# Performance work log

Hardware: AMD Instinct MI355X
Metric: run time of the kernel (lower is better)

Reference implementation:

```python
import jax, jax.numpy as jnp
import numpy as np

H = 16
D_MODEL = 1024
D_K = D_MODEL // H


def setup_inputs() -> dict:
    key = jax.random.key(0)
    ks = jax.random.split(key, 11)
    B, S = 2, 2048
    scale = 1.0 / np.sqrt(D_MODEL)
    inp = {
        "query": jax.random.normal(ks[0], (B, S, D_MODEL), dtype=jnp.float32),
        "key": jax.random.normal(ks[1], (B, S, D_MODEL), dtype=jnp.float32),
        "value": jax.random.normal(ks[2], (B, S, D_MODEL), dtype=jnp.float32),
        "Wq": jax.random.normal(ks[3], (D_MODEL, D_MODEL), dtype=jnp.float32) * scale,
        "bq": jnp.zeros((D_MODEL,), dtype=jnp.float32),
        "Wk": jax.random.normal(ks[4], (D_MODEL, D_MODEL), dtype=jnp.float32) * scale,
        "bk": jnp.zeros((D_MODEL,), dtype=jnp.float32),
        "Wv": jax.random.normal(ks[5], (D_MODEL, D_MODEL), dtype=jnp.float32) * scale,
        "bv": jnp.zeros((D_MODEL,), dtype=jnp.float32),
        "Wo": jax.random.normal(ks[6], (D_MODEL, D_MODEL), dtype=jnp.float32) * scale,
        "bo": jnp.zeros((D_MODEL,), dtype=jnp.float32),
    }
    return inp


def _mha(query, key, value, Wq, bq, Wk, bk, Wv, bv, Wo, bo):
    B, S, _ = query.shape
    # linear projections (torch nn.Linear: x @ W.T + b)
    q = query @ Wq.T + bq
    k = key @ Wk.T + bk
    v = value @ Wv.T + bv
    # split heads: [B, S, D] -> [B, H, S, d_k]
    q = q.reshape(B, S, H, D_K).transpose(0, 2, 1, 3)
    k = k.reshape(B, S, H, D_K).transpose(0, 2, 1, 3)
    v = v.reshape(B, S, H, D_K).transpose(0, 2, 1, 3)
    # scaled dot-product attention with manual stable softmax
    scores = jnp.einsum("bhqd,bhkd->bhqk", q, k) / jnp.sqrt(jnp.float32(D_K))
    stable = scores - jnp.max(scores, axis=-1, keepdims=True)
    e = jnp.exp(stable)
    attn = e / jnp.sum(e, axis=-1, keepdims=True)
    ctx = jnp.einsum("bhqk,bhkd->bhqd", attn, v)
    # merge heads and final projection
    ctx = ctx.transpose(0, 2, 1, 3).reshape(B, S, H * D_K)
    return ctx @ Wo.T + bo


def reference(query, key, value, Wq, bq, Wk, bk, Wv, bv, Wo, bo):
    return _mha(query, key, value, Wq, bq, Wk, bk, Wv, bv, Wo, bo)
```

## Files before the change

### kernel.cpp

```cpp
#include <hip/hip_runtime.h>


#define S_LEN 2048
#define BATCH 2
#define DM    1024
#define NH    16
#define DKH   64
#define BS    (BATCH * S_LEN)

typedef _Float16 f16x8 __attribute__((ext_vector_type(8)));
typedef _Float16 f16x4 __attribute__((ext_vector_type(4)));
typedef _Float16 f16x2 __attribute__((ext_vector_type(2)));
typedef __fp16   h16x2 __attribute__((ext_vector_type(2)));
typedef float    f32x4 __attribute__((ext_vector_type(4)));
typedef float    f32x16 __attribute__((ext_vector_type(16)));

__device__ __forceinline__ f16x2 pk_f16(float a, float b) {
  h16x2 r = __builtin_amdgcn_cvt_pkrtz(a, b);
  return __builtin_bit_cast(f16x2, r);
}

__device__ __forceinline__ void gld16(const void* g, void* l) {
  __builtin_amdgcn_global_load_lds(
      (const __attribute__((address_space(1))) void*)g,
      (__attribute__((address_space(3))) void*)l, 16, 0, 0);
}

__device__ __forceinline__ float fast_exp2(float x) {
#if __has_builtin(__builtin_amdgcn_exp2f)
  return __builtin_amdgcn_exp2f(x);
#else
  return exp2f(x);
#endif
}

__device__ __forceinline__ int swap23(int x) {
  return (x & ~12) | ((x & 4) << 1) | ((x & 8) >> 1);
}

__global__ __launch_bounds__(256) void cvt_all(
    const float* __restrict__ q, const float* __restrict__ k, const float* __restrict__ v,
    const float* __restrict__ wq, const float* __restrict__ wk,
    const float* __restrict__ wv, const float* __restrict__ wo,
    _Float16* __restrict__ xq, _Float16* __restrict__ xk, _Float16* __restrict__ xv,
    _Float16* __restrict__ w16)
{
  const int y = blockIdx.y;
  const float* src; _Float16* dst; int n;
  if (y == 0)      { src = q;  dst = xq; n = BS * DM; }
  else if (y == 1) { src = k;  dst = xk; n = BS * DM; }
  else if (y == 2) { src = v;  dst = xv; n = BS * DM; }
  else {
    src = (y == 3) ? wq : ((y == 4) ? wk : ((y == 5) ? wv : wo));
    dst = w16 + (size_t)(y - 3) * (DM * DM);
    n = DM * DM;
  }
  int i0 = (blockIdx.x * 256 + threadIdx.x) * 4;
  if (i0 < n) {
    float4 f = *(const float4*)(src + i0);
    f16x2 lo = pk_f16(f.x, f.y);
    f16x2 hi = pk_f16(f.z, f.w);
    f16x4 hh; hh[0] = lo[0]; hh[1] = lo[1]; hh[2] = hi[0]; hh[3] = hi[1];
    *(f16x4*)(dst + i0) = hh;
  }
}

template <typename OUT_T, bool VT>
__device__ __forceinline__ void gemm_core(
    const _Float16* __restrict__ A, const _Float16* __restrict__ W,
    const float* __restrict__ bias, OUT_T* __restrict__ out, float oscale)
{
  const int tid  = threadIdx.x;
  const int l    = tid & 63;
  const int wv   = tid >> 6;
  const int c    = l & 15, quad = l >> 4;
  const int m0   = blockIdx.y * 128, n0 = blockIdx.x * 128;
  const int wm   = wv & 1, wn = wv >> 1;
  __shared__ _Float16 sA[128 * 64];
  __shared__ _Float16 sB[128 * 64];

  const _Float16* gA[4]; const _Float16* gB[4];
#pragma unroll
  for (int p = 0; p < 4; ++p) {
    int s = tid + p * 256, r = s >> 3, g = (s & 7) ^ (r & 7);
    gA[p] = A + (size_t)(m0 + r) * DM + g * 8;
    gB[p] = W + (size_t)(n0 + r) * DM + g * 8;
  }
  const int cx = c & 7;

  f32x4 acc[4][4] = {};
  for (int k0 = 0; k0 < DM; k0 += 64) {
    __syncthreads();
#pragma unroll
    for (int p = 0; p < 4; ++p) {
      gld16(gA[p] + k0, sA + (tid + p * 256) * 8);
      gld16(gB[p] + k0, sB + (tid + p * 256) * 8);
    }
    __syncthreads();
#pragma unroll
    for (int ks = 0; ks < 2; ++ks) {
      f16x8 af[4], bf[4];
#pragma unroll
      for (int i = 0; i < 4; ++i)
        af[i] = *(const f16x8*)&sA[(wm * 64 + i * 16 + c) * 64 + ((ks * 4 + quad) ^ cx) * 8];
#pragma unroll
      for (int j = 0; j < 4; ++j)
        bf[j] = *(const f16x8*)&sB[(wn * 64 + j * 16 + c) * 64 + ((ks * 4 + quad) ^ cx) * 8];
#pragma unroll
      for (int i = 0; i < 4; ++i)
#pragma unroll
        for (int j = 0; j < 4; ++j)
          acc[i][j] = __builtin_amdgcn_mfma_f32_16x16x32_f16(af[i], bf[j], acc[i][j], 0, 0, 0);
    }
  }
  if constexpr (VT) {
#pragma unroll
    for (int j = 0; j < 4; ++j) {
      int col = n0 + wn * 64 + j * 16 + c;
      float bb = bias[col];
      int hh = col >> 6, dd = col & 63;
#pragma unroll
      for (int i = 0; i < 4; ++i) {
        int row = m0 + wm * 64 + i * 16 + quad * 4;
        int bb2 = row >> 11, ss = row & (S_LEN - 1);
        _Float16* dst = (_Float16*)out + ((size_t)(bb2 * NH + hh) * DKH + dd) * S_LEN + ss;
        f16x4 v4;
#pragma unroll
        for (int r = 0; r < 4; ++r) v4[r] = (_Float16)((acc[i][j][r] + bb) * oscale);
        *(f16x4*)dst = v4;
      }
    }
  } else {
#pragma unroll
    for (int j = 0; j < 4; ++j) {
      int col = n0 + wn * 64 + j * 16 + c;
      float bb = bias[col];
#pragma unroll
      for (int i = 0; i < 4; ++i) {
        int row = m0 + wm * 64 + i * 16 + quad * 4;
#pragma unroll
        for (int r = 0; r < 4; ++r) {
          float vv = (acc[i][j][r] + bb) * oscale;
          out[(size_t)(row + r) * DM + col] = (OUT_T)vv;
        }
      }
    }
  }
}

#define SC_Q (0.125f * 1.44269504088896340736f)

__global__ __launch_bounds__(256) void proj3(
    const _Float16* __restrict__ xq, const _Float16* __restrict__ xk,
    const _Float16* __restrict__ xv, const _Float16* __restrict__ w16,
    const float* __restrict__ bq, const float* __restrict__ bk, const float* __restrict__ bv,
    _Float16* __restrict__ Q, _Float16* __restrict__ K, _Float16* __restrict__ Vt)
{
  const int z = blockIdx.z;
  if (z == 2) {
    gemm_core<_Float16, true>(xv, w16 + (size_t)2 * DM * DM, bv, Vt, 1.0f);
  } else if (z == 0) {
    gemm_core<_Float16, false>(xq, w16, bq, Q, SC_Q);
  } else {
    gemm_core<_Float16, false>(xk, w16 + (size_t)DM * DM, bk, K, 1.0f);
  }
}

__global__ __launch_bounds__(256) void out_gemm(
    const _Float16* __restrict__ ctx, const _Float16* __restrict__ wo,
    const float* __restrict__ bo, float* __restrict__ out)
{
  gemm_core<float, false>(ctx, wo, bo, out, 1.0f);
}

__global__ __launch_bounds__(256, 2) void attn(
    const _Float16* __restrict__ Q, const _Float16* __restrict__ K,
    const _Float16* __restrict__ Vt, _Float16* __restrict__ ctx)
{
  const int tid = threadIdx.x;
  const int l   = tid & 63, wv = tid >> 6;
  const int lo5 = l & 31, hf = l >> 5;
  const int q0  = blockIdx.x * 128;
  const int bh  = blockIdx.y;
  const int b   = bh >> 4, hd = bh & 15;
  __shared__ _Float16 sK[3][64 * 64];
  __shared__ _Float16 sV[3][64 * 64];

  f16x8 qf[4];
  {
    const _Float16* Qg = Q + ((size_t)(b * S_LEN + q0 + wv * 32 + lo5)) * DM + hd * DKH + 8 * hf;
#pragma unroll
    for (int kc = 0; kc < 4; ++kc) qf[kc] = *(const f16x8*)(Qg + 16 * kc);
  }

  f32x16 o[2] = {};
  float l_part = 0.f;
  const f16x2 ones = {(_Float16)1.0f, (_Float16)1.0f};

  const _Float16* Kg0 = K + ((size_t)b * S_LEN) * DM + hd * DKH;
  const _Float16* Vg0 = Vt + ((size_t)bh * DKH) * S_LEN;

  const int sa = tid,       ra = sa >> 3, ba = (sa & 7) ^ (ra & 7);
  const int sb = tid + 256, rb = sb >> 3, bb = (sb & 7) ^ (rb & 7);
  const _Float16* gKa = Kg0 + (size_t)swap23(ra) * DM + ba * 8;
  const _Float16* gKb = Kg0 + (size_t)swap23(rb) * DM + bb * 8;
  const _Float16* gVa = Vg0 + (size_t)ra * S_LEN + ba * 8;
  const _Float16* gVb = Vg0 + (size_t)rb * S_LEN + bb * 8;
  const int rx = lo5 & 7;

#define STAGE(t, bf) do {                                   \
    const size_t k0s = (size_t)(t) * 64;                    \
    gld16(gKa + k0s * DM, sK[bf] + sa * 8);                 \
    gld16(gKb + k0s * DM, sK[bf] + sb * 8);                 \
    gld16(gVa + k0s,      sV[bf] + sa * 8);                 \
    gld16(gVb + k0s,      sV[bf] + sb * 8);                 \
  } while (0)

  STAGE(0, 0);
  STAGE(1, 1);

  int cur = 0;
  for (int kt = 0; kt < S_LEN / 64; ++kt) {
    if (kt == S_LEN / 64 - 1)
      asm volatile("s_waitcnt vmcnt(0)" ::: "memory");
    else
      asm volatile("s_waitcnt vmcnt(4)" ::: "memory");
    __builtin_amdgcn_s_barrier();
    if (kt < S_LEN / 64 - 2) {
      int nb = cur + 2; if (nb >= 3) nb -= 3;
      STAGE(kt + 2, nb);
    }

    const _Float16* sKc = sK[cur];
    const _Float16* sVc = sV[cur];

    f32x16 sAcc[2] = {};
    __builtin_amdgcn_s_setprio(1);
#pragma unroll
    for (int kb = 0; kb < 2; ++kb)
#pragma unroll
      for (int kc = 0; kc < 4; ++kc) {
        f16x8 kf = *(const f16x8*)&sKc[(32 * kb + lo5) * 64 + ((2 * kc + hf) ^ rx) * 8];
        sAcc[kb] = __builtin_amdgcn_mfma_f32_32x32x16_f16(kf, qf[kc], sAcc[kb], 0, 0, 0);
      }
    __builtin_amdgcn_s_setprio(0);

    f16x8 pPv[2][2];
#pragma unroll
    for (int kb = 0; kb < 2; ++kb)
#pragma unroll
      for (int half = 0; half < 2; ++half)
#pragma unroll
        for (int j2 = 0; j2 < 4; ++j2) {
          float p0 = fast_exp2(sAcc[kb][8 * half + 2 * j2]);
          float p1 = fast_exp2(sAcc[kb][8 * half + 2 * j2 + 1]);
          f16x2 pk = pk_f16(p0, p1);
          pPv[kb][half][2 * j2]     = pk[0];
          pPv[kb][half][2 * j2 + 1] = pk[1];
          l_part = __builtin_amdgcn_fdot2(__builtin_bit_cast(h16x2, pk),
                                          __builtin_bit_cast(h16x2, ones), l_part, false);
        }

    __builtin_amdgcn_s_setprio(1);
#pragma unroll
    for (int db = 0; db < 2; ++db)
#pragma unroll
      for (int kc2 = 0; kc2 < 4; ++kc2) {
        f16x8 vf = *(const f16x8*)&sVc[(32 * db + lo5) * 64 + ((2 * kc2 + hf) ^ rx) * 8];
        o[db] = __builtin_amdgcn_mfma_f32_32x32x16_f16(pPv[kc2 >> 1][kc2 & 1], vf, o[db], 0, 0, 0);
      }
    __builtin_amdgcn_s_setprio(0);

    cur = (cur == 2) ? 0 : cur + 1;
  }
#undef STAGE

  l_part += __shfl_xor(l_part, 32);
  float* lsum = (float*)&sK[0][0] + wv * 32;
  if (hf == 0) lsum[lo5] = l_part;
  float inv[16];
#pragma unroll
  for (int r = 0; r < 16; ++r) {
    int qq = 8 * (r >> 2) + 4 * hf + (r & 3);
    inv[r] = 1.0f / lsum[qq];
  }

  _Float16* Og = ctx + ((size_t)(b * S_LEN + q0 + wv * 32)) * DM + hd * DKH;
#pragma unroll
  for (int db = 0; db < 2; ++db)
#pragma unroll
    for (int r = 0; r < 16; ++r) {
      int qq = 8 * (r >> 2) + 4 * hf + (r & 3);
      Og[(size_t)qq * DM + 32 * db + lo5] = (_Float16)(o[db][r] * inv[r]);
    }
}

extern "C" void kernel_launch(void* const* d_in, const int* in_sizes, int n_in,
                              void* d_out, int out_size, void* d_ws, size_t ws_size,
                              hipStream_t stream)
{
  (void)in_sizes; (void)n_in; (void)out_size; (void)ws_size;
  const float* q  = (const float*)d_in[0];
  const float* k  = (const float*)d_in[1];
  const float* v  = (const float*)d_in[2];
  const float* wq = (const float*)d_in[3];
  const float* bq = (const float*)d_in[4];
  const float* wk = (const float*)d_in[5];
  const float* bk = (const float*)d_in[6];
  const float* wv = (const float*)d_in[7];
  const float* bv = (const float*)d_in[8];
  const float* wo = (const float*)d_in[9];
  const float* bo = (const float*)d_in[10];

  char* ws = (char*)d_ws;
  _Float16* XQ  = (_Float16*)(ws);
  _Float16* XK  = (_Float16*)(ws + (8u  << 20));
  _Float16* XV  = (_Float16*)(ws + (16u << 20));
  _Float16* W16 = (_Float16*)(ws + (24u << 20));
  _Float16* Qp  = (_Float16*)(ws + (32u << 20));
  _Float16* Kp  = (_Float16*)(ws + (40u << 20));
  _Float16* VT  = (_Float16*)(ws + (48u << 20));
  _Float16* CTX = XQ;
  float* out = (float*)d_out;

  cvt_all<<<dim3(4096, 7), 256, 0, stream>>>(q, k, v, wq, wk, wv, wo, XQ, XK, XV, W16);
  proj3<<<dim3(8, 32, 3), 256, 0, stream>>>(XQ, XK, XV, W16, bq, bk, bv, Qp, Kp, VT);
  attn<<<dim3(16, 32), 256, 0, stream>>>(Qp, Kp, VT, CTX);
  out_gemm<<<dim3(8, 32), 256, 0, stream>>>(CTX, W16 + (size_t)3 * DM * DM, bo, out);
}
```

Measured before the change: 229.7 us.

## Split attention key tiles across warp pairs and halve query block size

Each attention block now covers 64 queries instead of 128. The four waves are arranged as two query-halves times two key-halves, and each wave handles 32 of the 64 keys in every tile. The partial outputs and row sums of the two key-half waves are combined through shared memory at the end. This doubles the grid to 1024 blocks and raises the occupancy target, aiming to fill the 256 CUs better. In exchange, K/V tiles are loaded twice as often per query, the triple buffer becomes a double buffer with a full wait each iteration, and a reduction epilogue is added.

```diff
diff --git a/kernel.cpp b/kernel.cpp
--- a/kernel.cpp
+++ b/kernel.cpp
@@ -173,22 +173,23 @@
   gemm_core<float, false>(ctx, wo, bo, out, 1.0f);
 }
 
-__global__ __launch_bounds__(256, 2) void attn(
+__global__ __launch_bounds__(256, 4) void attn(
     const _Float16* __restrict__ Q, const _Float16* __restrict__ K,
     const _Float16* __restrict__ Vt, _Float16* __restrict__ ctx)
 {
   const int tid = threadIdx.x;
   const int l   = tid & 63, wv = tid >> 6;
   const int lo5 = l & 31, hf = l >> 5;
-  const int q0  = blockIdx.x * 128;
+  const int wq  = wv >> 1, wk = wv & 1;
+  const int q0  = blockIdx.x * 64;
   const int bh  = blockIdx.y;
   const int b   = bh >> 4, hd = bh & 15;
-  __shared__ _Float16 sK[3][64 * 64];
-  __shared__ _Float16 sV[3][64 * 64];
+  __shared__ _Float16 sK[2][64 * 64];
+  __shared__ _Float16 sV[2][64 * 64];
 
   f16x8 qf[4];
   {
-    const _Float16* Qg = Q + ((size_t)(b * S_LEN + q0 + wv * 32 + lo5)) * DM + hd * DKH + 8 * hf;
+    const _Float16* Qg = Q + ((size_t)(b * S_LEN + q0 + wq * 32 + lo5)) * DM + hd * DKH + 8 * hf;
 #pragma unroll
     for (int kc = 0; kc < 4; ++kc) qf[kc] = *(const f16x8*)(Qg + 16 * kc);
   }
@@ -217,82 +218,88 @@
   } while (0)
 
   STAGE(0, 0);
-  STAGE(1, 1);
-
-  int cur = 0;
-  for (int kt = 0; kt < S_LEN / 64; ++kt) {
-    if (kt == S_LEN / 64 - 1)
-      asm volatile("s_waitcnt vmcnt(0)" ::: "memory");
-    else
-      asm volatile("s_waitcnt vmcnt(4)" ::: "memory");
-    __builtin_amdgcn_s_barrier();
-    if (kt < S_LEN / 64 - 2) {
-      int nb = cur + 2; if (nb >= 3) nb -= 3;
-      STAGE(kt + 2, nb);
-    }
+  asm volatile("s_waitcnt vmcnt(0)" ::: "memory");
+  __builtin_amdgcn_s_barrier();
+
+  const int NT = S_LEN / 64;
+  for (int kt = 0; kt < NT; ++kt) {
+    const int cur = kt & 1;
+    if (kt + 1 < NT) STAGE(kt + 1, cur ^ 1);
 
     const _Float16* sKc = sK[cur];
     const _Float16* sVc = sV[cur];
 
-    f32x16 sAcc[2] = {};
+    f32x16 sAcc = {};
     __builtin_amdgcn_s_setprio(1);
 #pragma unroll
-    for (int kb = 0; kb < 2; ++kb)
-#pragma unroll
-      for (int kc = 0; kc < 4; ++kc) {
-        f16x8 kf = *(const f16x8*)&sKc[(32 * kb + lo5) * 64 + ((2 * kc + hf) ^ rx) * 8];
-        sAcc[kb] = __builtin_amdgcn_mfma_f32_32x32x16_f16(kf, qf[kc], sAcc[kb], 0, 0, 0);
-      }
+    for (int kc = 0; kc < 4; ++kc) {
+      f16x8 kf = *(const f16x8*)&sKc[(32 * wk + lo5) * 64 + ((2 * kc + hf) ^ rx) * 8];
+      sAcc = __builtin_amdgcn_mfma_f32_32x32x16_f16(kf, qf[kc], sAcc, 0, 0, 0);
+    }
     __builtin_amdgcn_s_setprio(0);
 
-    f16x8 pPv[2][2];
-#pragma unroll
-    for (int kb = 0; kb < 2; ++kb)
-#pragma unroll
-      for (int half = 0; half < 2; ++half)
-#pragma unroll
-        for (int j2 = 0; j2 < 4; ++j2) {
-          float p0 = fast_exp2(sAcc[kb][8 * half + 2 * j2]);
-          float p1 = fast_exp2(sAcc[kb][8 * half + 2 * j2 + 1]);
-          f16x2 pk = pk_f16(p0, p1);
-          pPv[kb][half][2 * j2]     = pk[0];
-          pPv[kb][half][2 * j2 + 1] = pk[1];
-          l_part = __builtin_amdgcn_fdot2(__builtin_bit_cast(h16x2, pk),
-                                          __builtin_bit_cast(h16x2, ones), l_part, false);
-        }
+    f16x8 pPv[2];
+#pragma unroll
+    for (int half = 0; half < 2; ++half)
+#pragma unroll
+      for (int j2 = 0; j2 < 4; ++j2) {
+        float p0 = fast_exp2(sAcc[8 * half + 2 * j2]);
+        float p1 = fast_exp2(sAcc[8 * half + 2 * j2 + 1]);
+        f16x2 pk = pk_f16(p0, p1);
+        pPv[half][2 * j2]     = pk[0];
+        pPv[half][2 * j2 + 1] = pk[1];
+        l_part = __builtin_amdgcn_fdot2(__builtin_bit_cast(h16x2, pk),
+                                        __builtin_bit_cast(h16x2, ones), l_part, false);
+      }
 
     __builtin_amdgcn_s_setprio(1);
 #pragma unroll
     for (int db = 0; db < 2; ++db)
 #pragma unroll
-      for (int kc2 = 0; kc2 < 4; ++kc2) {
+      for (int half = 0; half < 2; ++half) {
+        const int kc2 = 2 * wk + half;
         f16x8 vf = *(const f16x8*)&sVc[(32 * db + lo5) * 64 + ((2 * kc2 + hf) ^ rx) * 8];
-        o[db] = __builtin_amdgcn_mfma_f32_32x32x16_f16(pPv[kc2 >> 1][kc2 & 1], vf, o[db], 0, 0, 0);
+        o[db] = __builtin_amdgcn_mfma_f32_32x32x16_f16(pPv[half], vf, o[db], 0, 0, 0);
       }
     __builtin_amdgcn_s_setprio(0);
 
-    cur = (cur == 2) ? 0 : cur + 1;
+    if (kt + 1 < NT) {
+      asm volatile("s_waitcnt vmcnt(0)" ::: "memory");
+      __builtin_amdgcn_s_barrier();
+    }
   }
 #undef STAGE
 
+  __syncthreads();
+
   l_part += __shfl_xor(l_part, 32);
-  float* lsum = (float*)&sK[0][0] + wv * 32;
-  if (hf == 0) lsum[lo5] = l_part;
-  float inv[16];
-#pragma unroll
-  for (int r = 0; r < 16; ++r) {
-    int qq = 8 * (r >> 2) + 4 * hf + (r & 3);
-    inv[r] = 1.0f / lsum[qq];
-  }
-
-  _Float16* Og = ctx + ((size_t)(b * S_LEN + q0 + wv * 32)) * DM + hd * DKH;
-#pragma unroll
-  for (int db = 0; db < 2; ++db)
+  float* lbuf = (float*)&sK[0][0];
+  float* obuf = (float*)&sV[0][0];
+  if (hf == 0) lbuf[wv * 32 + lo5] = l_part;
+  if (wk == 1) {
+#pragma unroll
+    for (int db = 0; db < 2; ++db)
+#pragma unroll
+      for (int r = 0; r < 16; ++r) {
+        int qq = 8 * (r >> 2) + 4 * hf + (r & 3);
+        obuf[(wq * 32 + qq) * 64 + 32 * db + lo5] = o[db][r];
+      }
+  }
+  __syncthreads();
+
+  if (wk == 0) {
+    _Float16* Og = ctx + ((size_t)(b * S_LEN + q0 + wq * 32)) * DM + hd * DKH;
 #pragma unroll
     for (int r = 0; r < 16; ++r) {
       int qq = 8 * (r >> 2) + 4 * hf + (r & 3);
-      Og[(size_t)qq * DM + 32 * db + lo5] = (_Float16)(o[db][r] * inv[r]);
-    }
+      float inv = 1.0f / (lbuf[(2 * wq) * 32 + qq] + lbuf[(2 * wq + 1) * 32 + qq]);
+#pragma unroll
+      for (int db = 0; db < 2; ++db) {
+        float val = o[db][r] + obuf[(wq * 32 + qq) * 64 + 32 * db + lo5];
+        Og[(size_t)qq * DM + 32 * db + lo5] = (_Float16)(val * inv);
+      }
+    }
+  }
 }
 
 extern "C" void kernel_launch(void* const* d_in, const int* in_sizes, int n_in,
@@ -325,6 +332,6 @@
 
   cvt_all<<<dim3(4096, 7), 256, 0, stream>>>(q, k, v, wq, wk, wv, wo, XQ, XK, XV, W16);
   proj3<<<dim3(8, 32, 3), 256, 0, stream>>>(XQ, XK, XV, W16, bq, bk, bv, Qp, Kp, VT);
-  attn<<<dim3(16, 32), 256, 0, stream>>>(Qp, Kp, VT, CTX);
+  attn<<<dim3(32, 32), 256, 0, stream>>>(Qp, Kp, VT, CTX);
   out_gemm<<<dim3(8, 32), 256, 0, stream>>>(CTX, W16 + (size_t)3 * DM * DM, bo, out);
 }
```

Result: slower. 236.6 us (+3.0%).
